# Optimization experiments

Measured on AMD Instinct MI355X. Metric: run time of the kernel, lower is better.

## Reference

```python
import jax, jax.numpy as jnp
import numpy as np

GAMMA = 1.0 / 512.0  # RBF bandwidth, 1/d_feat


def _rbf_kernel(X, Z, gamma):
    # X: [N, d], Z: [M, d] -> K: [N, M], K[i,j] = exp(-gamma * ||x_i - z_j||^2)
    xn = jnp.sum(X * X, axis=1, keepdims=True)        # [N, 1]
    zn = jnp.sum(Z * Z, axis=1, keepdims=True).T      # [1, M]
    sq = xn + zn - 2.0 * (X @ Z.T)                    # [N, M]
    return jnp.exp(-gamma * jnp.maximum(sq, 0.0))


def setup_inputs() -> dict:
    key = jax.random.key(0)
    k1, k2, k3, k4, k5 = jax.random.split(key, 5)
    N, d, M = 8192, 512, 4096
    inputs = jax.random.normal(k1, (M, d), dtype=jnp.float32)
    X = jax.random.normal(k2, (N, d), dtype=jnp.float32)
    # SVM labels in {-1, +1}
    Y = jnp.where(jax.random.uniform(k3, (N, 1)) > 0.5, 1.0, -1.0).astype(jnp.float32)
    a = jax.random.normal(k4, (N, 1), dtype=jnp.float32) * 0.1
    b = jax.random.normal(k5, (1, 1), dtype=jnp.float32)
    return {"inputs": inputs, "X": X, "Y": Y, "a": a, "b": b}


def reference(inputs, X, Y, a, b):
    # K: [N, M]; weighted sum over support vectors N, then add bias, transpose.
    K = _rbf_kernel(X, inputs, GAMMA)                 # [N, M]
    s = jnp.sum(a * Y * K, axis=0)                    # [M]
    out = (s + b)                                     # [1, M] via broadcast with [1,1]
    return out.T                                      # [M, 1]
```

## Files before the change

### kernel.cpp

```cpp
#include <hip/hip_runtime.h>
#include <hip/hip_bf16.h>
#include <stdint.h>

#define GAMMA_F 0.001953125f
#define C2EXP (-0.0028179443441958f)

static constexpr int N_SV = 8192;
static constexpr int M_Q  = 4096;
static constexpr int DIM  = 512;

typedef __bf16 bf16x8 __attribute__((ext_vector_type(8)));
typedef float  f32x4  __attribute__((ext_vector_type(4)));

#define GLB const __attribute__((address_space(1))) void
#define LDS __attribute__((address_space(3))) void

__global__ __launch_bounds__(256) void svm_prep(
    const float* __restrict__ Z, const float* __restrict__ X,
    const float* __restrict__ Y, const float* __restrict__ a,
    const float* __restrict__ b,
    __bf16* __restrict__ Xb, __bf16* __restrict__ Zb,
    float* __restrict__ xn, float* __restrict__ zn, float* __restrict__ w,
    float* __restrict__ out)
{
    const int r = blockIdx.x * 4 + (threadIdx.x >> 6);
    const int t = threadIdx.x & 63;
    const float* src;
    __bf16* dst;
    if (r < N_SV) { src = X + (size_t)r * DIM; dst = Xb + (size_t)r * DIM; }
    else          { src = Z + (size_t)(r - N_SV) * DIM; dst = Zb + (size_t)(r - N_SV) * DIM; }

    const float4* row4 = (const float4*)src;
    float4 v0 = row4[t];
    float4 v1 = row4[t + 64];

    float s = v0.x*v0.x + v0.y*v0.y + v0.z*v0.z + v0.w*v0.w
            + v1.x*v1.x + v1.y*v1.y + v1.z*v1.z + v1.w*v1.w;

    __bf16 h0[4] = {(__bf16)v0.x, (__bf16)v0.y, (__bf16)v0.z, (__bf16)v0.w};
    __bf16 h1[4] = {(__bf16)v1.x, (__bf16)v1.y, (__bf16)v1.z, (__bf16)v1.w};
    uint2 b0, b1;
    __builtin_memcpy(&b0, h0, 8);
    __builtin_memcpy(&b1, h1, 8);
    ((uint2*)dst)[t]      = b0;
    ((uint2*)dst)[t + 64] = b1;

    #pragma unroll
    for (int o = 32; o > 0; o >>= 1) s += __shfl_xor(s, o);

    if (t == 0) {
        if (r < N_SV) { xn[r] = s; w[r] = a[r] * Y[r]; }
        else          { int m = r - N_SV; zn[m] = s; out[m] = b[0]; }
    }
}

__global__ __launch_bounds__(256) void svm_main(
    const __bf16* __restrict__ Xb, const __bf16* __restrict__ Zb,
    const float* __restrict__ xn, const float* __restrict__ zn,
    const float* __restrict__ w, float* __restrict__ out)
{
    __shared__ __bf16 As[2 * 128 * 32];
    __shared__ __bf16 Bs[2 * 128 * 32];

    const int tid  = threadIdx.x;
    const int lane = tid & 63;
    const int wid  = tid >> 6;
    const int wr   = wid >> 1;
    const int wc   = wid & 1;

    const int iBase = blockIdx.y * 128;
    const int jBase = blockIdx.x * 128;

    f32x4 acc[4][4];
    #pragma unroll
    for (int m = 0; m < 4; ++m)
        #pragma unroll
        for (int n = 0; n < 4; ++n)
            acc[m][n] = (f32x4)(0.0f);

    const int srow   = tid >> 2;
    const int schunk = (tid & 3) ^ ((tid >> 3) & 3);
    const int sce    = schunk * 8;

    const int lrow = lane & 15;
    const int rsw  = (lrow >> 1) & 3;
    const int lkb  = ((lane >> 4) ^ rsw) * 16;

    auto stage = [&](int buf, int k0) {
        #pragma unroll
        for (int q = 0; q < 2; ++q) {
            const int row = q * 64 + srow;
            const __bf16* sa = Xb + (size_t)(iBase + row) * DIM + k0 + sce;
            __builtin_amdgcn_global_load_lds((GLB*)sa,
                (LDS*)((char*)As + buf * 8192 + q * 4096 + tid * 16), 16, 0, 0);
            const __bf16* sb = Zb + (size_t)(jBase + row) * DIM + k0 + sce;
            __builtin_amdgcn_global_load_lds((GLB*)sb,
                (LDS*)((char*)Bs + buf * 8192 + q * 4096 + tid * 16), 16, 0, 0);
        }
    };

    stage(0, 0);
    __syncthreads();

    #pragma unroll
    for (int kt = 0; kt < 16; ++kt) {
        const int buf = kt & 1;
        if (kt < 15) stage(buf ^ 1, (kt + 1) * 32);

        bf16x8 af[4], bfr[4];
        #pragma unroll
        for (int m = 0; m < 4; ++m)
            af[m] = *(const bf16x8*)((const char*)As + buf * 8192
                        + (wr * 64 + m * 16 + lrow) * 64 + lkb);
        #pragma unroll
        for (int n = 0; n < 4; ++n)
            bfr[n] = *(const bf16x8*)((const char*)Bs + buf * 8192
                        + (wc * 64 + n * 16 + lrow) * 64 + lkb);

        #pragma unroll
        for (int m = 0; m < 4; ++m)
            #pragma unroll
            for (int n = 0; n < 4; ++n)
                acc[m][n] = __builtin_amdgcn_mfma_f32_16x16x32_bf16(
                    af[m], bfr[n], acc[m][n], 0, 0, 0);

        __syncthreads();
    }

    const int rg   = lane >> 4;
    const int lcol = lane & 15;

    float wv[16], xv[16];
    #pragma unroll
    for (int m = 0; m < 4; ++m)
        #pragma unroll
        for (int r = 0; r < 4; ++r) {
            const int i = iBase + wr * 64 + m * 16 + rg * 4 + r;
            wv[m * 4 + r] = w[i];
            xv[m * 4 + r] = xn[i];
        }

    #pragma unroll
    for (int n = 0; n < 4; ++n) {
        const int j = jBase + wc * 64 + n * 16 + lcol;
        const float znj = zn[j];
        float cs = 0.0f;
        #pragma unroll
        for (int m = 0; m < 4; ++m)
            #pragma unroll
            for (int r = 0; r < 4; ++r) {
                float d = xv[m * 4 + r] + znj - 2.0f * acc[m][n][r];
                d = fmaxf(d, 0.0f);
                cs += wv[m * 4 + r] * exp2f(C2EXP * d);
            }
        cs += __shfl_xor(cs, 16);
        cs += __shfl_xor(cs, 32);
        if (lane < 16) atomicAdd(out + j, cs);
    }
}

extern "C" void kernel_launch(void* const* d_in, const int* in_sizes, int n_in,
                              void* d_out, int out_size, void* d_ws, size_t ws_size,
                              hipStream_t stream)
{
    const float* Z = (const float*)d_in[0];
    const float* X = (const float*)d_in[1];
    const float* Y = (const float*)d_in[2];
    const float* a = (const float*)d_in[3];
    const float* b = (const float*)d_in[4];
    float* out = (float*)d_out;

    char* ws = (char*)d_ws;
    __bf16* Xb = (__bf16*)ws;
    __bf16* Zb = (__bf16*)(ws + 8ull * 1024 * 1024);
    float*  xn = (float*)(ws + 12ull * 1024 * 1024);
    float*  zn = xn + N_SV;
    float*  w  = zn + M_Q;

    svm_prep<<<(N_SV + M_Q) / 4, 256, 0, stream>>>(Z, X, Y, a, b, Xb, Zb, xn, zn, w, out);
    svm_main<<<dim3(M_Q / 128, N_SV / 128), 256, 0, stream>>>(Xb, Zb, xn, zn, w, out);
}
```

Baseline: 136.8 us.

## Enlarge GEMM tile to 256x256 with 8 waves and split-phase LDS pipeline

```diff
diff --git a/kernel.cpp b/kernel.cpp
--- a/kernel.cpp
+++ b/kernel.cpp
@@ -2,7 +2,6 @@
 #include <hip/hip_bf16.h>
 #include <stdint.h>
 
-#define GAMMA_F 0.001953125f
 #define C2EXP (-0.0028179443441958f)
 
 static constexpr int N_SV = 8192;
@@ -54,108 +53,134 @@
     }
 }
 
-__global__ __launch_bounds__(256) void svm_main(
+__global__ __launch_bounds__(512, 2) void svm_main(
     const __bf16* __restrict__ Xb, const __bf16* __restrict__ Zb,
     const float* __restrict__ xn, const float* __restrict__ zn,
     const float* __restrict__ w, float* __restrict__ out)
 {
-    __shared__ __bf16 As[2 * 128 * 32];
-    __shared__ __bf16 Bs[2 * 128 * 32];
+    __shared__ char Sh[65536];
 
     const int tid  = threadIdx.x;
     const int lane = tid & 63;
     const int wid  = tid >> 6;
-    const int wr   = wid >> 1;
-    const int wc   = wid & 1;
-
-    const int iBase = blockIdx.y * 128;
-    const int jBase = blockIdx.x * 128;
-
-    f32x4 acc[4][4];
-    #pragma unroll
-    for (int m = 0; m < 4; ++m)
+    const int wr   = wid >> 2;
+    const int wc   = wid & 3;
+
+    const int iBase = blockIdx.y * 256;
+    const int jBase = blockIdx.x * 256;
+
+    f32x4 acc[8][4];
+    #pragma unroll
+    for (int m = 0; m < 8; ++m)
         #pragma unroll
         for (int n = 0; n < 4; ++n)
             acc[m][n] = (f32x4)(0.0f);
 
-    const int srow   = tid >> 2;
-    const int schunk = (tid & 3) ^ ((tid >> 3) & 3);
-    const int sce    = schunk * 8;
-
-    const int lrow = lane & 15;
-    const int rsw  = (lrow >> 1) & 3;
-    const int lkb  = ((lane >> 4) ^ rsw) * 16;
-
-    auto stage = [&](int buf, int k0) {
-        #pragma unroll
-        for (int q = 0; q < 2; ++q) {
-            const int row = q * 64 + srow;
-            const __bf16* sa = Xb + (size_t)(iBase + row) * DIM + k0 + sce;
-            __builtin_amdgcn_global_load_lds((GLB*)sa,
-                (LDS*)((char*)As + buf * 8192 + q * 4096 + tid * 16), 16, 0, 0);
-            const __bf16* sb = Zb + (size_t)(jBase + row) * DIM + k0 + sce;
-            __builtin_amdgcn_global_load_lds((GLB*)sb,
-                (LDS*)((char*)Bs + buf * 8192 + q * 4096 + tid * 16), 16, 0, 0);
+    auto stage = [&](const __bf16* Mb, int rowBase, int t, int op) {
+        char* dst0 = (char*)Sh + ((t & 1) * 32768) + op * 16384 + tid * 16;
+        const __bf16* src0 = Mb
+            + (size_t)(rowBase + (lane & 15)) * DIM + t * 32 + (lane >> 4) * 8;
+        #pragma unroll
+        for (int s = 0; s < 2; ++s) {
+            const __bf16* src = src0 + (size_t)((s * 8 + wid) * 16) * DIM;
+            __builtin_amdgcn_global_load_lds((GLB*)src, (LDS*)(dst0 + s * 8192),
+                                             16, 0, 0);
         }
     };
 
-    stage(0, 0);
-    __syncthreads();
-
-    #pragma unroll
-    for (int kt = 0; kt < 16; ++kt) {
-        const int buf = kt & 1;
-        if (kt < 15) stage(buf ^ 1, (kt + 1) * 32);
-
-        bf16x8 af[4], bfr[4];
-        #pragma unroll
-        for (int m = 0; m < 4; ++m)
-            af[m] = *(const bf16x8*)((const char*)As + buf * 8192
-                        + (wr * 64 + m * 16 + lrow) * 64 + lkb);
+    stage(Xb, iBase, 0, 0);
+    stage(Zb, jBase, 0, 1);
+    stage(Zb, jBase, 1, 1);
+    asm volatile("s_waitcnt vmcnt(2)" ::: "memory");
+    __builtin_amdgcn_s_barrier();
+
+    bf16x8 af[4], bfr[4];
+
+    #pragma unroll
+    for (int t = 0; t < 16; ++t) {
+        const int buf = t & 1;
+        const char* Ab = (const char*)Sh + buf * 32768 + lane * 16;
+
+        #pragma unroll
+        for (int m = 0; m < 4; ++m)
+            af[m] = *(const bf16x8*)(Ab + (wr * 8 + m) * 1024);
         #pragma unroll
         for (int n = 0; n < 4; ++n)
-            bfr[n] = *(const bf16x8*)((const char*)Bs + buf * 8192
-                        + (wc * 64 + n * 16 + lrow) * 64 + lkb);
-
+            bfr[n] = *(const bf16x8*)(Ab + 16384 + (wc * 4 + n) * 1024);
+        if (t + 1 < 16) stage(Xb, iBase, t + 1, 0);
+        __builtin_amdgcn_s_barrier();
+        asm volatile("s_waitcnt lgkmcnt(0)" ::: "memory");
+        __builtin_amdgcn_sched_barrier(0);
+        __builtin_amdgcn_s_setprio(1);
         #pragma unroll
         for (int m = 0; m < 4; ++m)
             #pragma unroll
             for (int n = 0; n < 4; ++n)
                 acc[m][n] = __builtin_amdgcn_mfma_f32_16x16x32_bf16(
                     af[m], bfr[n], acc[m][n], 0, 0, 0);
-
-        __syncthreads();
+        __builtin_amdgcn_s_setprio(0);
+        __builtin_amdgcn_s_barrier();
+
+        #pragma unroll
+        for (int m = 0; m < 4; ++m)
+            af[m] = *(const bf16x8*)(Ab + (wr * 8 + 4 + m) * 1024);
+        if (t + 2 < 16) stage(Zb, jBase, t + 2, 1);
+        __builtin_amdgcn_s_barrier();
+        asm volatile("s_waitcnt lgkmcnt(0)" ::: "memory");
+        __builtin_amdgcn_sched_barrier(0);
+        __builtin_amdgcn_s_setprio(1);
+        #pragma unroll
+        for (int m = 0; m < 4; ++m)
+            #pragma unroll
+            for (int n = 0; n < 4; ++n)
+                acc[4 + m][n] = __builtin_amdgcn_mfma_f32_16x16x32_bf16(
+                    af[m], bfr[n], acc[4 + m][n], 0, 0, 0);
+        __builtin_amdgcn_s_setprio(0);
+
+        if (t < 14) {
+            asm volatile("s_waitcnt vmcnt(2)" ::: "memory");
+            __builtin_amdgcn_s_barrier();
+        } else if (t == 14) {
+            asm volatile("s_waitcnt vmcnt(0)" ::: "memory");
+            __builtin_amdgcn_s_barrier();
+        }
     }
 
     const int rg   = lane >> 4;
     const int lcol = lane & 15;
 
-    float wv[16], xv[16];
-    #pragma unroll
-    for (int m = 0; m < 4; ++m)
+    float znv[4];
+    #pragma unroll
+    for (int n = 0; n < 4; ++n)
+        znv[n] = zn[jBase + wc * 64 + n * 16 + lcol];
+
+    float cs[4] = {0.f, 0.f, 0.f, 0.f};
+    #pragma unroll
+    for (int m = 0; m < 8; ++m) {
+        float wv[4], xv[4];
         #pragma unroll
         for (int r = 0; r < 4; ++r) {
-            const int i = iBase + wr * 64 + m * 16 + rg * 4 + r;
-            wv[m * 4 + r] = w[i];
-            xv[m * 4 + r] = xn[i];
+            const int i = iBase + wr * 128 + m * 16 + rg * 4 + r;
+            wv[r] = w[i];
+            xv[r] = xn[i];
         }
+        #pragma unroll
+        for (int n = 0; n < 4; ++n)
+            #pragma unroll
+            for (int r = 0; r < 4; ++r) {
+                float d = xv[r] + znv[n] - 2.0f * acc[m][n][r];
+                d = fmaxf(d, 0.0f);
+                cs[n] += wv[r] * exp2f(C2EXP * d);
+            }
+    }
 
     #pragma unroll
     for (int n = 0; n < 4; ++n) {
         const int j = jBase + wc * 64 + n * 16 + lcol;
-        const float znj = zn[j];
-        float cs = 0.0f;
-        #pragma unroll
-        for (int m = 0; m < 4; ++m)
-            #pragma unroll
-            for (int r = 0; r < 4; ++r) {
-                float d = xv[m * 4 + r] + znj - 2.0f * acc[m][n][r];
-                d = fmaxf(d, 0.0f);
-                cs += wv[m * 4 + r] * exp2f(C2EXP * d);
-            }
-        cs += __shfl_xor(cs, 16);
-        cs += __shfl_xor(cs, 32);
-        if (lane < 16) atomicAdd(out + j, cs);
+        float c = cs[n];
+        c += __shfl_xor(c, 16);
+        c += __shfl_xor(c, 32);
+        if (lane < 16) atomicAdd(out + j, c);
     }
 }
 
@@ -178,5 +203,5 @@
     float*  w  = zn + M_Q;
 
     svm_prep<<<(N_SV + M_Q) / 4, 256, 0, stream>>>(Z, X, Y, a, b, Xb, Zb, xn, zn, w, out);
-    svm_main<<<dim3(M_Q / 128, N_SV / 128), 256, 0, stream>>>(Xb, Zb, xn, zn, w, out);
+    svm_main<<<dim3(M_Q / 256, N_SV / 256), 512, 0, stream>>>(Xb, Zb, xn, zn, w, out);
 }
```

Measured after the change: 119.9 us. 1.14x faster.
